# Kernel optimization log

Hardware: AMD Instinct MI355X
Metric: run time of the kernel (lower is better)

## Reference

```python
import jax, jax.numpy as jnp
import numpy as np
from jax import lax

C_OUT = 32   # out_capsules[0]
D_OUT = 8    # out_capsules[1]
ROUTING_ITERS = 3
EPS = 1e-8


def squash(s):
    # squash over capsule-channel axis c (dim 1 of B c d h w)
    n2 = jnp.sum(s * s, axis=1, keepdims=True)
    return s * (n2 / (1.0 + n2)) / jnp.sqrt(n2 + EPS)


def setup_inputs() -> dict:
    key = jax.random.key(0)
    k1, k2 = jax.random.split(key)
    x = jax.random.normal(k1, (8, 16, 8, 96, 96), dtype=jnp.float32)
    # torch Conv3d weight layout: (out_ch, in_ch, kD, kH, kW); scaled ~ kaiming-ish
    w_conv = jax.random.normal(k2, (C_OUT * D_OUT, 16, 1, 3, 3), dtype=jnp.float32) * 0.05
    return {"x": x, "w_conv": w_conv}


def reference(x, w_conv):
    # Conv3d, no bias, valid padding, stride 1, kernel (1,3,3)
    u = lax.conv_general_dilated(
        x, w_conv, window_strides=(1, 1, 1), padding='VALID',
        dimension_numbers=('NCDHW', 'OIDHW', 'NCDHW'))  # (B, c*d, D, h, w)
    B, _, D, h, w = u.shape
    # rearrange 'B (c d) D h w -> B c D d h w'
    u = u.reshape(B, C_OUT, D_OUT, D, h, w).transpose(0, 1, 3, 2, 4, 5)

    b = jnp.zeros((B, D, D_OUT, h, w), dtype=u.dtype)
    s = None
    for _ in range(ROUTING_ITERS):
        # softmax_3d: exp normalized over (d, h, w), keeping D
        e = jnp.exp(b)
        c = e / jnp.sum(e, axis=(2, 3, 4), keepdims=True)
        s = jnp.einsum('BDdhw,BcDdhw->Bcdhw', c, u)
        b = b + jnp.einsum('BcDdhw,Bcdhw->BDdhw', u, squash(s))
    return s
```

## Files before the change

kernel.cpp:

```cpp
#include <hip/hip_runtime.h>
#include <math.h>

#define CIN   16
#define DDEP  8
#define HIN   96
#define WIN   96
#define HOUT  94
#define WOUT  94
#define HW    (HOUT*WOUT)
#define CH    256
#define DCAP  8
#define KTOT  (CIN*9)
#define KTILES 5
#define APAD  168
#define EPSQ  1e-8f

#define B_ELEMS ((size_t)8*DDEP*DCAP*HW)
#define WFRAG_ELEMS ((size_t)KTILES*16*64*8)
#define BLK_PER_B (94*12)
#define NBLK ((size_t)8*BLK_PER_B)
#define A_TILE_BYTES ((size_t)64*APAD*2)
#define A_TILE_V4 (A_TILE_BYTES/16)
#define AC_BYTES (NBLK*A_TILE_BYTES)
#define VSITES (DCAP*HW)
#define NBLK2  277
#define G_BYTES ((size_t)8*VSITES*36*4)

typedef __attribute__((ext_vector_type(8))) short bf16x8;
typedef __attribute__((ext_vector_type(4))) float f32x4;

__device__ __forceinline__ ushort f2bf(float f) {
    unsigned u = __float_as_uint(f);
    return (ushort)((u + 0x7FFFu + ((u >> 16) & 1u)) >> 16);
}
__device__ __forceinline__ float bf2f(ushort h) {
    return __uint_as_float(((unsigned)h) << 16);
}

__global__ __launch_bounds__(64) void build_wfrag(
    const float* __restrict__ w, ushort* __restrict__ w_hi, ushort* __restrict__ w_lo)
{
    const int lane = threadIdx.x;
    const int nt = blockIdx.x, kt = blockIdx.y;
    const int n  = nt*16 + (lane & 15);
    const int kb = kt*32 + (lane >> 4)*8;
    size_t off = (((size_t)kt*16 + nt)*64 + lane)*8;
    for (int j = 0; j < 8; ++j) {
        int k = kb + j;
        float v = (k < KTOT) ? w[(size_t)n*KTOT + k] : 0.f;
        ushort hi = f2bf(v);
        float  r  = v - bf2f(hi);
        ushort lo = f2bf(r);
        w_hi[off + j] = hi; w_lo[off + j] = lo;
    }
}

__global__ __launch_bounds__(256) void zreduce(
    const float* __restrict__ Zp, float* __restrict__ Z, int dst, int count)
{
    const int bd = blockIdx.x;
    const float* p = Zp + (size_t)bd * count;
    float s = 0.f;
    for (int i = threadIdx.x; i < count; i += 256) s += p[i];
    #pragma unroll
    for (int off = 1; off < 64; off <<= 1) s += __shfl_xor(s, off);
    __shared__ float ps[4];
    if ((threadIdx.x & 63) == 0) ps[threadIdx.x >> 6] = s;
    __syncthreads();
    if (threadIdx.x == 0) Z[dst + bd] = ps[0] + ps[1] + ps[2] + ps[3];
}

template<int MODE>
__device__ __forceinline__ void routing_epilogue(
    const f32x4 (&acc)[4][4], const int t, const int wx, const int h0, const int bb,
    const float (*cms)[8], const float* invZ,
    float (*n2s)[8][8], float (*dbs)[8][8][8], float (*sout)[8],
    float* __restrict__ bws, float* __restrict__ Zp, float* __restrict__ out)
{
    const int w0 = wx*8;
    const int wv = t >> 6, lane = t & 63;
    const int m16 = lane & 15, quad = lane >> 4;
    const int d   = m16 & 7;
    const int Dq  = quad >> 1;
    const int wih = quad & 1;

    float svv[4][4];
    {
        float cmw[4][4];
        if (MODE == 0) {
            const float inv = 1.0f / (float)(DCAP * HW);
            #pragma unroll
            for (int mt = 0; mt < 4; ++mt)
                #pragma unroll
                for (int r = 0; r < 4; ++r) cmw[mt][r] = inv;
        } else {
            #pragma unroll
            for (int mt = 0; mt < 4; ++mt) {
                int D = mt*2 + Dq;
                float iz = invZ[D];
                #pragma unroll
                for (int r = 0; r < 4; ++r) cmw[mt][r] = cms[D*8 + d][wih*4 + r] * iz;
            }
        }
        #pragma unroll
        for (int nt = 0; nt < 4; ++nt)
            #pragma unroll
            for (int r = 0; r < 4; ++r) {
                float partial = 0.f;
                #pragma unroll
                for (int mt = 0; mt < 4; ++mt) partial += cmw[mt][r]*acc[mt][nt][r];
                partial += __shfl_xor(partial, 32);
                svv[nt][r] = partial;
            }
    }

    if (MODE == 2) {
        if (quad < 2) {
            #pragma unroll
            for (int nt = 0; nt < 4; ++nt) {
                int ch = wv*64 + nt*16 + m16;
                #pragma unroll
                for (int r = 0; r < 4; ++r) sout[ch][wih*4 + r] = svv[nt][r];
            }
        }
        __syncthreads();
        for (int i = t; i < 1024; i += 256) {
            int c2 = i >> 2, wip = i & 3;
            int w = w0 + wip*2;
            if (w + 1 < WOUT) {
                float2 v2 = { sout[c2][wip*2], sout[c2][wip*2 + 1] };
                *(float2*)&out[((size_t)bb*CH + c2)*HW + (size_t)h0*WOUT + w] = v2;
            }
        }
        return;
    }

    float p2[4];
    #pragma unroll
    for (int r = 0; r < 4; ++r) {
        float s2 = 0.f;
        #pragma unroll
        for (int nt = 0; nt < 4; ++nt) s2 += svv[nt][r]*svv[nt][r];
        p2[r] = s2;
    }
    #pragma unroll
    for (int r = 0; r < 4; ++r) p2[r] += __shfl_xor(p2[r], 8);
    if (quad < 2 && m16 < 8) {
        #pragma unroll
        for (int r = 0; r < 4; ++r) n2s[wv][m16][quad*4 + r] = p2[r];
    }
    __syncthreads();
    float fac[4];
    #pragma unroll
    for (int r = 0; r < 4; ++r) {
        int wi = wih*4 + r;
        float n2 = n2s[0][d][wi] + n2s[1][d][wi] + n2s[2][d][wi] + n2s[3][d][wi];
        fac[r] = (n2 / (1.f + n2)) / sqrtf(n2 + EPSQ);
    }
    float qv[4][4];
    #pragma unroll
    for (int mt = 0; mt < 4; ++mt)
        #pragma unroll
        for (int r = 0; r < 4; ++r) {
            float sum = 0.f;
            #pragma unroll
            for (int nt = 0; nt < 4; ++nt)
                sum += acc[mt][nt][r] * (svv[nt][r] * fac[r]);
            qv[mt][r] = sum;
        }
    #pragma unroll
    for (int mt = 0; mt < 4; ++mt)
        #pragma unroll
        for (int r = 0; r < 4; ++r) qv[mt][r] += __shfl_xor(qv[mt][r], 8);
    if (m16 < 8) {
        #pragma unroll
        for (int mt = 0; mt < 4; ++mt) {
            int D = mt*2 + Dq;
            #pragma unroll
            for (int r = 0; r < 4; ++r) dbs[wv][D][m16][wih*4 + r] = qv[mt][r];
        }
    }
    __syncthreads();
    {
        int Dd = t >> 2, wip = t & 3;
        int D = Dd >> 3, d2 = Dd & 7;
        int w = w0 + wip*2;
        float ez = 0.f;
        if (w + 1 < WOUT) {
            int wi = wip*2;
            float2 add;
            add.x = dbs[0][D][d2][wi]   + dbs[1][D][d2][wi]
                  + dbs[2][D][d2][wi]   + dbs[3][D][d2][wi];
            add.y = dbs[0][D][d2][wi+1] + dbs[1][D][d2][wi+1]
                  + dbs[2][D][d2][wi+1] + dbs[3][D][d2][wi+1];
            float2* bp = (float2*)&bws[((size_t)bb*64 + Dd)*HW + (size_t)h0*WOUT + w];
            if (MODE != 0) { float2 old = *bp; add.x += old.x; add.y += old.y; }
            *bp = add;
            ez = expf(add.x) + expf(add.y);
        }
        #pragma unroll
        for (int off = 1; off < 32; off <<= 1) ez += __shfl_xor(ez, off);
        if ((t & 31) == 0)
            Zp[((size_t)bb*8 + D)*BLK_PER_B + h0*12 + wx] = ez;
    }
}

template<int MODE, int AC, bool GW>
__global__ __launch_bounds__(256, 2) void conv_mfma_route(
    const float* __restrict__ x,
    const ushort* __restrict__ w_hi, const ushort* __restrict__ w_lo,
    float* __restrict__ bws, const float* __restrict__ Z,
    float* __restrict__ Zp, float* __restrict__ out,
    float* __restrict__ Ac, float* __restrict__ Gm)
{
    const int t  = threadIdx.x;
    const int wx = blockIdx.x, h0 = blockIdx.y, bb = blockIdx.z;
    const int w0 = wx*8;
    const size_t blk = ((size_t)bb*94 + h0)*12 + wx;

    __shared__ __align__(16) ushort a_hi[64][APAD];
    __shared__ float  cms[64][8];
    __shared__ float  invZ[8];
    __shared__ union {
        float patch[CIN][DDEP][3][10];
        struct { float n2s[4][8][8];
                 float dbs[4][8][8][8]; } ep;
        float sout[256][8];
        float gst[4][16][36];
    } ov;

    if (MODE != 0) {
        if (t < 8) invZ[t] = 1.0f / Z[(MODE == 2 ? 64 : 0) + bb*8 + t];
        for (int v = t; v < 512; v += 256) {
            int Dd = v >> 3, wi = v & 7;
            int w = w0 + wi;
            float bv = (w < WOUT) ? bws[((size_t)bb*64 + Dd)*HW + (size_t)h0*WOUT + w] : 0.f;
            cms[Dd][wi] = expf(bv);
        }
    }

    if (AC == 2) {
        const float4* src = (const float4*)Ac + blk*A_TILE_V4;
        float4* dst = (float4*)&a_hi[0][0];
        for (int i = t; i < A_TILE_V4; i += 256) dst[i] = src[i];
        __syncthreads();
    } else {
        for (int i = t; i < CIN*DDEP*3*10; i += 256) {
            int ci = i / 240, rem = i - ci*240;
            int D  = rem / 30, rem2 = rem - D*30;
            int kh = rem2 / 10, col = rem2 - kh*10;
            int xc = w0 + col; if (xc > 95) xc = 95;
            ov.patch[ci][D][kh][col] =
                x[(((size_t)(bb*CIN + ci)*DDEP + D)*HIN + (h0+kh))*WIN + xc];
        }
        __syncthreads();

        {
            const int site = t >> 2, kg = t & 3;
            const int D = site >> 3, wi = site & 7;
            #pragma unroll
            for (int u2 = 0; u2 < 18; ++u2) {
                int k0 = kg*36 + u2*2;
                int ci0 = k0/9, r0 = k0 - ci0*9, kh0 = r0/3, kw0 = r0 - kh0*3;
                int k1 = k0 + 1;
                int ci1 = k1/9, r1 = k1 - ci1*9, kh1 = r1/3, kw1 = r1 - kh1*3;
                unsigned lo = f2bf(ov.patch[ci0][D][kh0][wi+kw0]);
                unsigned hi = f2bf(ov.patch[ci1][D][kh1][wi+kw1]);
                *(unsigned*)&a_hi[site][k0] = lo | (hi << 16);
            }
            if (t < 64) {
                #pragma unroll
                for (int kk = KTOT; kk < KTILES*32; kk += 2)
                    *(unsigned*)&a_hi[t][kk] = 0u;
            }
        }
        __syncthreads();
    }

    const int wv = t >> 6, lane = t & 63;
    const int m16 = lane & 15, quad = lane >> 4;
    const int Dq = quad >> 1, wih = quad & 1;
    f32x4 acc[4][4];
    #pragma unroll
    for (int mt = 0; mt < 4; ++mt)
        #pragma unroll
        for (int nt = 0; nt < 4; ++nt)
            acc[mt][nt] = (f32x4){0.f, 0.f, 0.f, 0.f};

    #pragma unroll
    for (int kt = 0; kt < KTILES; ++kt) {
        bf16x8 ah[4];
        #pragma unroll
        for (int mt = 0; mt < 4; ++mt)
            ah[mt] = *(const bf16x8*)&a_hi[mt*16 + m16][kt*32 + quad*8];
        #pragma unroll
        for (int nt = 0; nt < 4; ++nt) {
            size_t off = (((size_t)kt*16 + (wv*4 + nt))*64 + lane)*8;
            bf16x8 bh = *(const bf16x8*)&w_hi[off];
            bf16x8 bl = *(const bf16x8*)&w_lo[off];
            #pragma unroll
            for (int mt = 0; mt < 4; ++mt) {
                acc[mt][nt] = __builtin_amdgcn_mfma_f32_16x16x32_bf16(ah[mt], bh, acc[mt][nt], 0, 0, 0);
                acc[mt][nt] = __builtin_amdgcn_mfma_f32_16x16x32_bf16(ah[mt], bl, acc[mt][nt], 0, 0, 0);
            }
        }
    }

    if (AC == 1) {
        float4* dst = (float4*)Ac + blk*A_TILE_V4;
        const float4* src = (const float4*)&a_hi[0][0];
        for (int i = t; i < A_TILE_V4; i += 256) dst[i] = src[i];
    }

    routing_epilogue<MODE>(acc, t, wx, h0, bb, cms, invZ,
                           ov.ep.n2s, ov.ep.dbs, ov.sout, bws, Zp, out);

    if constexpr (GW) {
        const int c3 = m16 >> 3;
        const int dL = m16 & 7;
        __syncthreads();
        #pragma unroll
        for (int r = 0; r < 4; ++r) {
            const int rq = r >> 1;
            float G36[36];
            #pragma unroll
            for (int j = 0; j < 36; ++j) G36[j] = 0.f;
            #pragma unroll
            for (int nt = 0; nt < 4; ++nt) {
                float u8[8];
                #pragma unroll
                for (int mt = 0; mt < 4; ++mt) {
                    float own = acc[mt][nt][r];
                    float oth = __shfl_xor(own, 32);
                    if (Dq == 0) { u8[mt*2]   = own; u8[mt*2+1] = oth; }
                    else         { u8[mt*2+1] = own; u8[mt*2]   = oth; }
                }
                if (Dq == rq) {
                    int idx = 0;
                    #pragma unroll
                    for (int D = 0; D < 8; ++D)
                        #pragma unroll
                        for (int Dp = D; Dp < 8; ++Dp) {
                            G36[idx] += u8[D]*u8[Dp];
                            ++idx;
                        }
                }
            }
            if (Dq == rq) {
                #pragma unroll
                for (int j = 0; j < 36; ++j) G36[j] += __shfl_xor(G36[j], 8);
                if (c3 == 0) {
                    #pragma unroll
                    for (int j = 0; j < 36; ++j) ov.gst[wv][dL*2 + wih][j] = G36[j];
                }
            }
            __syncthreads();
            for (int idx2 = t; idx2 < 16*36; idx2 += 256) {
                int sidx = idx2 / 36, j = idx2 - sidx*36;
                int dd = sidx >> 1, wh = sidx & 1;
                int w = w0 + wh*4 + r;
                if (w < WOUT) {
                    float gv = ov.gst[0][sidx][j] + ov.gst[1][sidx][j]
                             + ov.gst[2][sidx][j] + ov.gst[3][sidx][j];
                    size_t gsite = ((size_t)(bb*DCAP + dd)*HOUT + h0)*WOUT + w;
                    Gm[gsite*36 + j] = gv;
                }
            }
            __syncthreads();
        }
    }
}

__global__ __launch_bounds__(256) void gram_route(
    const float* __restrict__ Gm, float* __restrict__ bws,
    const float* __restrict__ Z, float* __restrict__ Zp)
{
    const int k = blockIdx.x, bb = blockIdx.y;
    const int t = threadIdx.x;
    const int local = k*256 + t;
    const bool valid = local < VSITES;
    float ez[8];
    #pragma unroll
    for (int D = 0; D < 8; ++D) ez[D] = 0.f;
    if (valid) {
        const int d  = local / HW;
        const int r2 = local - d*HW;
        float bv[8], cm[8];
        #pragma unroll
        for (int D = 0; D < 8; ++D) {
            bv[D] = bws[((size_t)(bb*64 + D*8 + d))*HW + r2];
            cm[D] = expf(bv[D]) * (1.0f / Z[bb*8 + D]);
        }
        float g[36];
        const float4* gp = (const float4*)(Gm + (size_t)(bb*VSITES + local)*36);
        #pragma unroll
        for (int q = 0; q < 9; ++q) {
            float4 v = gp[q];
            g[q*4+0] = v.x; g[q*4+1] = v.y; g[q*4+2] = v.z; g[q*4+3] = v.w;
        }
        float tD[8];
        #pragma unroll
        for (int D = 0; D < 8; ++D) tD[D] = 0.f;
        {
            int idx = 0;
            #pragma unroll
            for (int D = 0; D < 8; ++D)
                #pragma unroll
                for (int Dp = D; Dp < 8; ++Dp) {
                    float gv = g[idx]; ++idx;
                    tD[D] += cm[Dp] * gv;
                    if (Dp != D) tD[Dp] += cm[D] * gv;
                }
        }
        float n2 = 0.f;
        #pragma unroll
        for (int D = 0; D < 8; ++D) n2 += cm[D] * tD[D];
        float fac = (n2 / (1.f + n2)) / sqrtf(n2 + EPSQ);
        #pragma unroll
        for (int D = 0; D < 8; ++D) {
            float nb = bv[D] + fac * tD[D];
            bws[((size_t)(bb*64 + D*8 + d))*HW + r2] = nb;
            ez[D] = expf(nb);
        }
    }
    #pragma unroll
    for (int D = 0; D < 8; ++D)
        #pragma unroll
        for (int off = 1; off < 64; off <<= 1) ez[D] += __shfl_xor(ez[D], off);
    __shared__ float ps[4][8];
    if ((t & 63) == 0) {
        #pragma unroll
        for (int D = 0; D < 8; ++D) ps[t >> 6][D] = ez[D];
    }
    __syncthreads();
    if (t < 8)
        Zp[((size_t)bb*8 + t)*NBLK2 + k] = ps[0][t] + ps[1][t] + ps[2][t] + ps[3][t];
}

extern "C" void kernel_launch(void* const* d_in, const int* in_sizes, int n_in,
                              void* d_out, int out_size, void* d_ws, size_t ws_size,
                              hipStream_t stream)
{
    (void)in_sizes; (void)n_in; (void)out_size;
    const float* x     = (const float*)d_in[0];
    const float* wconv = (const float*)d_in[1];
    float* out = (float*)d_out;

    float*  bws  = (float*)d_ws;
    float*  Z    = bws + B_ELEMS;
    float*  Zp   = Z + 128;
    ushort* w_hi = (ushort*)(Zp + 64*BLK_PER_B);
    ushort* w_lo = w_hi + WFRAG_ELEMS;
    size_t  base = (size_t)((char*)(w_lo + WFRAG_ELEMS) - (char*)d_ws);
    size_t  goff = (base + 255) & ~(size_t)255;
    float*  Gm   = (float*)((char*)d_ws + goff);
    size_t  aoff = (goff + G_BYTES + 255) & ~(size_t)255;
    float*  Ac   = (float*)((char*)d_ws + aoff);
    const bool haveG = ws_size >= goff + G_BYTES;
    const bool haveA = ws_size >= aoff + AC_BYTES;

    const dim3 grid(12, 94, 8);
    build_wfrag<<<dim3(16, KTILES), 64, 0, stream>>>(wconv, w_hi, w_lo);
    if (haveG && haveA) {
        conv_mfma_route<0, 1, true ><<<grid, 256, 0, stream>>>(x, w_hi, w_lo, bws, Z, Zp, out, Ac, Gm);
        zreduce<<<64, 256, 0, stream>>>(Zp, Z, 0, BLK_PER_B);
        gram_route<<<dim3(NBLK2, 8), 256, 0, stream>>>(Gm, bws, Z, Zp);
        zreduce<<<64, 256, 0, stream>>>(Zp, Z, 64, NBLK2);
        conv_mfma_route<2, 2, false><<<grid, 256, 0, stream>>>(x, w_hi, w_lo, bws, Z, Zp, out, Ac, nullptr);
    } else if (haveG) {
        conv_mfma_route<0, 0, true ><<<grid, 256, 0, stream>>>(x, w_hi, w_lo, bws, Z, Zp, out, nullptr, Gm);
        zreduce<<<64, 256, 0, stream>>>(Zp, Z, 0, BLK_PER_B);
        gram_route<<<dim3(NBLK2, 8), 256, 0, stream>>>(Gm, bws, Z, Zp);
        zreduce<<<64, 256, 0, stream>>>(Zp, Z, 64, NBLK2);
        conv_mfma_route<2, 0, false><<<grid, 256, 0, stream>>>(x, w_hi, w_lo, bws, Z, Zp, out, nullptr, nullptr);
    } else {
        conv_mfma_route<0, 0, false><<<grid, 256, 0, stream>>>(x, w_hi, w_lo, bws, Z, Zp, out, nullptr, nullptr);
        zreduce<<<64, 256, 0, stream>>>(Zp, Z, 0, BLK_PER_B);
        conv_mfma_route<1, 0, false><<<grid, 256, 0, stream>>>(x, w_hi, w_lo, bws, Z, Zp, out, nullptr, nullptr);
        zreduce<<<64, 256, 0, stream>>>(Zp, Z, 64, BLK_PER_B);
        conv_mfma_route<2, 0, false><<<grid, 256, 0, stream>>>(x, w_hi, w_lo, bws, Z, Zp, out, nullptr, nullptr);
    }
}
```

Before: 592.0 us.

## Route all iterations through Gram matrices and pre-convert input to bf16

Pre-converts x to bf16 once in a separate kernel so both conv passes load half-width patches. The first conv pass now only computes per-site 8x8 Gram matrices (no routing epilogue or A-tile caching), and iteration one's routing update is moved into a templated gram_route with uniform coupling. A dedicated final conv kernel computes the weighted sum output, and occupancy is raised to 4 blocks per SM. The workspace-size fallbacks are removed, so the path assumes enough workspace for xb and Gm.

After: 1.401 ms. 2.37x slower.

```diff
diff --git a/kernel.cpp b/kernel.cpp
--- a/kernel.cpp
+++ b/kernel.cpp
@@ -17,13 +17,9 @@
 
 #define B_ELEMS ((size_t)8*DDEP*DCAP*HW)
 #define WFRAG_ELEMS ((size_t)KTILES*16*64*8)
-#define BLK_PER_B (94*12)
-#define NBLK ((size_t)8*BLK_PER_B)
-#define A_TILE_BYTES ((size_t)64*APAD*2)
-#define A_TILE_V4 (A_TILE_BYTES/16)
-#define AC_BYTES (NBLK*A_TILE_BYTES)
 #define VSITES (DCAP*HW)
 #define NBLK2  277
+#define XN ((size_t)8*CIN*DDEP*HIN*WIN)
 #define G_BYTES ((size_t)8*VSITES*36*4)
 
 typedef __attribute__((ext_vector_type(8))) short bf16x8;
@@ -55,6 +51,17 @@
     }
 }
 
+__global__ __launch_bounds__(256) void xconvert(
+    const float* __restrict__ x, ushort* __restrict__ xb)
+{
+    size_t i = (size_t)blockIdx.x*256 + threadIdx.x;
+    if (i*4 >= XN) return;
+    float4 v = ((const float4*)x)[i];
+    ushort4 o;
+    o.x = f2bf(v.x); o.y = f2bf(v.y); o.z = f2bf(v.z); o.w = f2bf(v.w);
+    ((ushort4*)xb)[i] = o;
+}
+
 __global__ __launch_bounds__(256) void zreduce(
     const float* __restrict__ Zp, float* __restrict__ Z, int dst, int count)
 {
@@ -70,212 +77,54 @@
     if (threadIdx.x == 0) Z[dst + bd] = ps[0] + ps[1] + ps[2] + ps[3];
 }
 
-template<int MODE>
-__device__ __forceinline__ void routing_epilogue(
-    const f32x4 (&acc)[4][4], const int t, const int wx, const int h0, const int bb,
-    const float (*cms)[8], const float* invZ,
-    float (*n2s)[8][8], float (*dbs)[8][8][8], float (*sout)[8],
-    float* __restrict__ bws, float* __restrict__ Zp, float* __restrict__ out)
-{
-    const int w0 = wx*8;
-    const int wv = t >> 6, lane = t & 63;
-    const int m16 = lane & 15, quad = lane >> 4;
-    const int d   = m16 & 7;
-    const int Dq  = quad >> 1;
-    const int wih = quad & 1;
-
-    float svv[4][4];
-    {
-        float cmw[4][4];
-        if (MODE == 0) {
-            const float inv = 1.0f / (float)(DCAP * HW);
-            #pragma unroll
-            for (int mt = 0; mt < 4; ++mt)
-                #pragma unroll
-                for (int r = 0; r < 4; ++r) cmw[mt][r] = inv;
-        } else {
-            #pragma unroll
-            for (int mt = 0; mt < 4; ++mt) {
-                int D = mt*2 + Dq;
-                float iz = invZ[D];
-                #pragma unroll
-                for (int r = 0; r < 4; ++r) cmw[mt][r] = cms[D*8 + d][wih*4 + r] * iz;
-            }
-        }
-        #pragma unroll
-        for (int nt = 0; nt < 4; ++nt)
-            #pragma unroll
-            for (int r = 0; r < 4; ++r) {
-                float partial = 0.f;
-                #pragma unroll
-                for (int mt = 0; mt < 4; ++mt) partial += cmw[mt][r]*acc[mt][nt][r];
-                partial += __shfl_xor(partial, 32);
-                svv[nt][r] = partial;
-            }
-    }
-
-    if (MODE == 2) {
-        if (quad < 2) {
-            #pragma unroll
-            for (int nt = 0; nt < 4; ++nt) {
-                int ch = wv*64 + nt*16 + m16;
-                #pragma unroll
-                for (int r = 0; r < 4; ++r) sout[ch][wih*4 + r] = svv[nt][r];
-            }
-        }
-        __syncthreads();
-        for (int i = t; i < 1024; i += 256) {
-            int c2 = i >> 2, wip = i & 3;
-            int w = w0 + wip*2;
-            if (w + 1 < WOUT) {
-                float2 v2 = { sout[c2][wip*2], sout[c2][wip*2 + 1] };
-                *(float2*)&out[((size_t)bb*CH + c2)*HW + (size_t)h0*WOUT + w] = v2;
-            }
-        }
-        return;
-    }
-
-    float p2[4];
-    #pragma unroll
-    for (int r = 0; r < 4; ++r) {
-        float s2 = 0.f;
-        #pragma unroll
-        for (int nt = 0; nt < 4; ++nt) s2 += svv[nt][r]*svv[nt][r];
-        p2[r] = s2;
-    }
-    #pragma unroll
-    for (int r = 0; r < 4; ++r) p2[r] += __shfl_xor(p2[r], 8);
-    if (quad < 2 && m16 < 8) {
-        #pragma unroll
-        for (int r = 0; r < 4; ++r) n2s[wv][m16][quad*4 + r] = p2[r];
-    }
-    __syncthreads();
-    float fac[4];
-    #pragma unroll
-    for (int r = 0; r < 4; ++r) {
-        int wi = wih*4 + r;
-        float n2 = n2s[0][d][wi] + n2s[1][d][wi] + n2s[2][d][wi] + n2s[3][d][wi];
-        fac[r] = (n2 / (1.f + n2)) / sqrtf(n2 + EPSQ);
-    }
-    float qv[4][4];
-    #pragma unroll
-    for (int mt = 0; mt < 4; ++mt)
-        #pragma unroll
-        for (int r = 0; r < 4; ++r) {
-            float sum = 0.f;
-            #pragma unroll
-            for (int nt = 0; nt < 4; ++nt)
-                sum += acc[mt][nt][r] * (svv[nt][r] * fac[r]);
-            qv[mt][r] = sum;
-        }
-    #pragma unroll
-    for (int mt = 0; mt < 4; ++mt)
-        #pragma unroll
-        for (int r = 0; r < 4; ++r) qv[mt][r] += __shfl_xor(qv[mt][r], 8);
-    if (m16 < 8) {
-        #pragma unroll
-        for (int mt = 0; mt < 4; ++mt) {
-            int D = mt*2 + Dq;
-            #pragma unroll
-            for (int r = 0; r < 4; ++r) dbs[wv][D][m16][wih*4 + r] = qv[mt][r];
-        }
-    }
-    __syncthreads();
-    {
-        int Dd = t >> 2, wip = t & 3;
-        int D = Dd >> 3, d2 = Dd & 7;
-        int w = w0 + wip*2;
-        float ez = 0.f;
-        if (w + 1 < WOUT) {
-            int wi = wip*2;
-            float2 add;
-            add.x = dbs[0][D][d2][wi]   + dbs[1][D][d2][wi]
-                  + dbs[2][D][d2][wi]   + dbs[3][D][d2][wi];
-            add.y = dbs[0][D][d2][wi+1] + dbs[1][D][d2][wi+1]
-                  + dbs[2][D][d2][wi+1] + dbs[3][D][d2][wi+1];
-            float2* bp = (float2*)&bws[((size_t)bb*64 + Dd)*HW + (size_t)h0*WOUT + w];
-            if (MODE != 0) { float2 old = *bp; add.x += old.x; add.y += old.y; }
-            *bp = add;
-            ez = expf(add.x) + expf(add.y);
-        }
-        #pragma unroll
-        for (int off = 1; off < 32; off <<= 1) ez += __shfl_xor(ez, off);
-        if ((t & 31) == 0)
-            Zp[((size_t)bb*8 + D)*BLK_PER_B + h0*12 + wx] = ez;
-    }
-}
-
-template<int MODE, int AC, bool GW>
-__global__ __launch_bounds__(256, 2) void conv_mfma_route(
-    const float* __restrict__ x,
+__global__ __launch_bounds__(256, 4) void conv_g(
+    const ushort* __restrict__ xb,
     const ushort* __restrict__ w_hi, const ushort* __restrict__ w_lo,
-    float* __restrict__ bws, const float* __restrict__ Z,
-    float* __restrict__ Zp, float* __restrict__ out,
-    float* __restrict__ Ac, float* __restrict__ Gm)
+    float* __restrict__ Gm)
 {
     const int t  = threadIdx.x;
     const int wx = blockIdx.x, h0 = blockIdx.y, bb = blockIdx.z;
     const int w0 = wx*8;
-    const size_t blk = ((size_t)bb*94 + h0)*12 + wx;
 
     __shared__ __align__(16) ushort a_hi[64][APAD];
-    __shared__ float  cms[64][8];
-    __shared__ float  invZ[8];
     __shared__ union {
-        float patch[CIN][DDEP][3][10];
-        struct { float n2s[4][8][8];
-                 float dbs[4][8][8][8]; } ep;
-        float sout[256][8];
-        float gst[4][16][36];
+        ushort patchb[CIN][DDEP][3][10];
+        float  gst[2][4][16][36];
     } ov;
 
-    if (MODE != 0) {
-        if (t < 8) invZ[t] = 1.0f / Z[(MODE == 2 ? 64 : 0) + bb*8 + t];
-        for (int v = t; v < 512; v += 256) {
-            int Dd = v >> 3, wi = v & 7;
-            int w = w0 + wi;
-            float bv = (w < WOUT) ? bws[((size_t)bb*64 + Dd)*HW + (size_t)h0*WOUT + w] : 0.f;
-            cms[Dd][wi] = expf(bv);
-        }
-    }
-
-    if (AC == 2) {
-        const float4* src = (const float4*)Ac + blk*A_TILE_V4;
-        float4* dst = (float4*)&a_hi[0][0];
-        for (int i = t; i < A_TILE_V4; i += 256) dst[i] = src[i];
-        __syncthreads();
-    } else {
-        for (int i = t; i < CIN*DDEP*3*10; i += 256) {
-            int ci = i / 240, rem = i - ci*240;
-            int D  = rem / 30, rem2 = rem - D*30;
-            int kh = rem2 / 10, col = rem2 - kh*10;
-            int xc = w0 + col; if (xc > 95) xc = 95;
-            ov.patch[ci][D][kh][col] =
-                x[(((size_t)(bb*CIN + ci)*DDEP + D)*HIN + (h0+kh))*WIN + xc];
-        }
-        __syncthreads();
-
-        {
-            const int site = t >> 2, kg = t & 3;
-            const int D = site >> 3, wi = site & 7;
-            #pragma unroll
-            for (int u2 = 0; u2 < 18; ++u2) {
-                int k0 = kg*36 + u2*2;
-                int ci0 = k0/9, r0 = k0 - ci0*9, kh0 = r0/3, kw0 = r0 - kh0*3;
-                int k1 = k0 + 1;
-                int ci1 = k1/9, r1 = k1 - ci1*9, kh1 = r1/3, kw1 = r1 - kh1*3;
-                unsigned lo = f2bf(ov.patch[ci0][D][kh0][wi+kw0]);
-                unsigned hi = f2bf(ov.patch[ci1][D][kh1][wi+kw1]);
-                *(unsigned*)&a_hi[site][k0] = lo | (hi << 16);
-            }
-            if (t < 64) {
-                #pragma unroll
-                for (int kk = KTOT; kk < KTILES*32; kk += 2)
-                    *(unsigned*)&a_hi[t][kk] = 0u;
-            }
-        }
-        __syncthreads();
-    }
+    for (int i = t; i < CIN*DDEP*3*5; i += 256) {
+        int ci = i / 120, rem = i - ci*120;
+        int D  = rem / 15, r2 = rem - D*15;
+        int kh = r2 / 5, uc = r2 - kh*5;
+        int xc = w0 + uc*2;
+        const ushort* row = xb + (((size_t)(bb*CIN + ci)*DDEP + D)*HIN + (h0+kh))*WIN;
+        unsigned v;
+        if (xc + 1 < WIN) v = *(const unsigned*)&row[xc];
+        else { unsigned e = row[95]; v = e | (e << 16); }
+        *(unsigned*)&ov.patchb[ci][D][kh][uc*2] = v;
+    }
+    __syncthreads();
+
+    {
+        const int site = t >> 2, kg = t & 3;
+        const int D = site >> 3, wi = site & 7;
+        #pragma unroll
+        for (int u2 = 0; u2 < 18; ++u2) {
+            int k0 = kg*36 + u2*2;
+            int ci0 = k0/9, r0 = k0 - ci0*9, kh0 = r0/3, kw0 = r0 - kh0*3;
+            int k1 = k0 + 1;
+            int ci1 = k1/9, r1 = k1 - ci1*9, kh1 = r1/3, kw1 = r1 - kh1*3;
+            unsigned lo = ov.patchb[ci0][D][kh0][wi+kw0];
+            unsigned hi = ov.patchb[ci1][D][kh1][wi+kw1];
+            *(unsigned*)&a_hi[site][k0] = lo | (hi << 16);
+        }
+        if (t < 64) {
+            #pragma unroll
+            for (int kk = KTOT; kk < KTILES*32; kk += 2)
+                *(unsigned*)&a_hi[t][kk] = 0u;
+        }
+    }
+    __syncthreads();
 
     const int wv = t >> 6, lane = t & 63;
     const int m16 = lane & 15, quad = lane >> 4;
@@ -306,22 +155,12 @@
         }
     }
 
-    if (AC == 1) {
-        float4* dst = (float4*)Ac + blk*A_TILE_V4;
-        const float4* src = (const float4*)&a_hi[0][0];
-        for (int i = t; i < A_TILE_V4; i += 256) dst[i] = src[i];
-    }
-
-    routing_epilogue<MODE>(acc, t, wx, h0, bb, cms, invZ,
-                           ov.ep.n2s, ov.ep.dbs, ov.sout, bws, Zp, out);
-
-    if constexpr (GW) {
-        const int c3 = m16 >> 3;
-        const int dL = m16 & 7;
-        __syncthreads();
-        #pragma unroll
-        for (int r = 0; r < 4; ++r) {
-            const int rq = r >> 1;
+    const int dL = m16 & 7;
+    #pragma unroll
+    for (int rp = 0; rp < 2; ++rp) {
+        #pragma unroll
+        for (int rb = 0; rb < 2; ++rb) {
+            const int r = rp*2 + rb;
             float G36[36];
             #pragma unroll
             for (int j = 0; j < 36; ++j) G36[j] = 0.f;
@@ -332,45 +171,43 @@
                 for (int mt = 0; mt < 4; ++mt) {
                     float own = acc[mt][nt][r];
                     float oth = __shfl_xor(own, 32);
-                    if (Dq == 0) { u8[mt*2]   = own; u8[mt*2+1] = oth; }
-                    else         { u8[mt*2+1] = own; u8[mt*2]   = oth; }
+                    u8[mt*2]     = (Dq == 0) ? own : oth;
+                    u8[mt*2 + 1] = (Dq == 0) ? oth : own;
                 }
-                if (Dq == rq) {
-                    int idx = 0;
+                int idx = 0;
+                #pragma unroll
+                for (int D = 0; D < 8; ++D)
                     #pragma unroll
-                    for (int D = 0; D < 8; ++D)
-                        #pragma unroll
-                        for (int Dp = D; Dp < 8; ++Dp) {
-                            G36[idx] += u8[D]*u8[Dp];
-                            ++idx;
-                        }
-                }
-            }
-            if (Dq == rq) {
+                    for (int Dp = D; Dp < 8; ++Dp) {
+                        G36[idx] += u8[D]*u8[Dp];
+                        ++idx;
+                    }
+            }
+            #pragma unroll
+            for (int j = 0; j < 36; ++j) G36[j] += __shfl_xor(G36[j], 8);
+            if (Dq == 0 && m16 < 8) {
                 #pragma unroll
-                for (int j = 0; j < 36; ++j) G36[j] += __shfl_xor(G36[j], 8);
-                if (c3 == 0) {
-                    #pragma unroll
-                    for (int j = 0; j < 36; ++j) ov.gst[wv][dL*2 + wih][j] = G36[j];
-                }
-            }
-            __syncthreads();
-            for (int idx2 = t; idx2 < 16*36; idx2 += 256) {
-                int sidx = idx2 / 36, j = idx2 - sidx*36;
-                int dd = sidx >> 1, wh = sidx & 1;
-                int w = w0 + wh*4 + r;
-                if (w < WOUT) {
-                    float gv = ov.gst[0][sidx][j] + ov.gst[1][sidx][j]
-                             + ov.gst[2][sidx][j] + ov.gst[3][sidx][j];
-                    size_t gsite = ((size_t)(bb*DCAP + dd)*HOUT + h0)*WOUT + w;
-                    Gm[gsite*36 + j] = gv;
-                }
-            }
-            __syncthreads();
-        }
-    }
-}
-
+                for (int j = 0; j < 36; ++j) ov.gst[rb][wv][dL*2 + wih][j] = G36[j];
+            }
+        }
+        __syncthreads();
+        for (int idx2 = t; idx2 < 2*16*36; idx2 += 256) {
+            int rb = idx2 / 576, rem = idx2 - rb*576;
+            int sidx = rem / 36, j = rem - sidx*36;
+            int dd = sidx >> 1, wh = sidx & 1;
+            int w = w0 + wh*4 + rp*2 + rb;
+            if (w < WOUT) {
+                float gv = ov.gst[rb][0][sidx][j] + ov.gst[rb][1][sidx][j]
+                         + ov.gst[rb][2][sidx][j] + ov.gst[rb][3][sidx][j];
+                size_t gsite = ((size_t)(bb*DCAP + dd)*HOUT + h0)*WOUT + w;
+                Gm[gsite*36 + j] = gv;
+            }
+        }
+        if (rp == 0) __syncthreads();
+    }
+}
+
+template<int ITER>
 __global__ __launch_bounds__(256) void gram_route(
     const float* __restrict__ Gm, float* __restrict__ bws,
     const float* __restrict__ Z, float* __restrict__ Zp)
@@ -379,17 +216,23 @@
     const int t = threadIdx.x;
     const int local = k*256 + t;
     const bool valid = local < VSITES;
-    float ez[8];
-    #pragma unroll
-    for (int D = 0; D < 8; ++D) ez[D] = 0.f;
+    float ez8[8];
+    #pragma unroll
+    for (int D = 0; D < 8; ++D) ez8[D] = 0.f;
     if (valid) {
         const int d  = local / HW;
         const int r2 = local - d*HW;
         float bv[8], cm[8];
-        #pragma unroll
-        for (int D = 0; D < 8; ++D) {
-            bv[D] = bws[((size_t)(bb*64 + D*8 + d))*HW + r2];
-            cm[D] = expf(bv[D]) * (1.0f / Z[bb*8 + D]);
+        if (ITER == 1) {
+            const float inv = 1.0f / (float)(DCAP * HW);
+            #pragma unroll
+            for (int D = 0; D < 8; ++D) { bv[D] = 0.f; cm[D] = inv; }
+        } else {
+            #pragma unroll
+            for (int D = 0; D < 8; ++D) {
+                bv[D] = bws[((size_t)(bb*64 + D*8 + d))*HW + r2];
+                cm[D] = expf(bv[D]) * (1.0f / Z[bb*8 + D]);
+            }
         }
         float g[36];
         const float4* gp = (const float4*)(Gm + (size_t)(bb*VSITES + local)*36);
@@ -420,28 +263,158 @@
         for (int D = 0; D < 8; ++D) {
             float nb = bv[D] + fac * tD[D];
             bws[((size_t)(bb*64 + D*8 + d))*HW + r2] = nb;
-            ez[D] = expf(nb);
+            ez8[D] = expf(nb);
         }
     }
     #pragma unroll
     for (int D = 0; D < 8; ++D)
         #pragma unroll
-        for (int off = 1; off < 64; off <<= 1) ez[D] += __shfl_xor(ez[D], off);
+        for (int off = 1; off < 64; off <<= 1) ez8[D] += __shfl_xor(ez8[D], off);
     __shared__ float ps[4][8];
     if ((t & 63) == 0) {
         #pragma unroll
-        for (int D = 0; D < 8; ++D) ps[t >> 6][D] = ez[D];
+        for (int D = 0; D < 8; ++D) ps[t >> 6][D] = ez8[D];
     }
     __syncthreads();
     if (t < 8)
         Zp[((size_t)bb*8 + t)*NBLK2 + k] = ps[0][t] + ps[1][t] + ps[2][t] + ps[3][t];
+}
+
+__global__ __launch_bounds__(256, 4) void conv_s(
+    const ushort* __restrict__ xb,
+    const ushort* __restrict__ w_hi, const ushort* __restrict__ w_lo,
+    const float* __restrict__ bws, const float* __restrict__ Z,
+    float* __restrict__ out)
+{
+    const int t  = threadIdx.x;
+    const int wx = blockIdx.x, h0 = blockIdx.y, bb = blockIdx.z;
+    const int w0 = wx*8;
+
+    __shared__ __align__(16) ushort a_hi[64][APAD];
+    __shared__ float  cms[64][8];
+    __shared__ float  invZ[8];
+    __shared__ union {
+        ushort patchb[CIN][DDEP][3][10];
+        float  sout[256][8];
+    } ov;
+
+    if (t < 8) invZ[t] = 1.0f / Z[64 + bb*8 + t];
+    for (int v = t; v < 512; v += 256) {
+        int Dd = v >> 3, wi = v & 7;
+        int w = w0 + wi;
+        float bv = (w < WOUT) ? bws[((size_t)bb*64 + Dd)*HW + (size_t)h0*WOUT + w] : 0.f;
+        cms[Dd][wi] = expf(bv);
+    }
+    for (int i = t; i < CIN*DDEP*3*5; i += 256) {
+        int ci = i / 120, rem = i - ci*120;
+        int D  = rem / 15, r2 = rem - D*15;
+        int kh = r2 / 5, uc = r2 - kh*5;
+        int xc = w0 + uc*2;
+        const ushort* row = xb + (((size_t)(bb*CIN + ci)*DDEP + D)*HIN + (h0+kh))*WIN;
+        unsigned v;
+        if (xc + 1 < WIN) v = *(const unsigned*)&row[xc];
+        else { unsigned e = row[95]; v = e | (e << 16); }
+        *(unsigned*)&ov.patchb[ci][D][kh][uc*2] = v;
+    }
+    __syncthreads();
+
+    {
+        const int site = t >> 2, kg = t & 3;
+        const int D = site >> 3, wi = site & 7;
+        #pragma unroll
+        for (int u2 = 0; u2 < 18; ++u2) {
+            int k0 = kg*36 + u2*2;
+            int ci0 = k0/9, r0 = k0 - ci0*9, kh0 = r0/3, kw0 = r0 - kh0*3;
+            int k1 = k0 + 1;
+            int ci1 = k1/9, r1 = k1 - ci1*9, kh1 = r1/3, kw1 = r1 - kh1*3;
+            unsigned lo = ov.patchb[ci0][D][kh0][wi+kw0];
+            unsigned hi = ov.patchb[ci1][D][kh1][wi+kw1];
+            *(unsigned*)&a_hi[site][k0] = lo | (hi << 16);
+        }
+        if (t < 64) {
+            #pragma unroll
+            for (int kk = KTOT; kk < KTILES*32; kk += 2)
+                *(unsigned*)&a_hi[t][kk] = 0u;
+        }
+    }
+    __syncthreads();
+
+    const int wv = t >> 6, lane = t & 63;
+    const int m16 = lane & 15, quad = lane >> 4;
+    f32x4 acc[4][4];
+    #pragma unroll
+    for (int mt = 0; mt < 4; ++mt)
+        #pragma unroll
+        for (int nt = 0; nt < 4; ++nt)
+            acc[mt][nt] = (f32x4){0.f, 0.f, 0.f, 0.f};
+
+    #pragma unroll
+    for (int kt = 0; kt < KTILES; ++kt) {
+        bf16x8 ah[4];
+        #pragma unroll
+        for (int mt = 0; mt < 4; ++mt)
+            ah[mt] = *(const bf16x8*)&a_hi[mt*16 + m16][kt*32 + quad*8];
+        #pragma unroll
+        for (int nt = 0; nt < 4; ++nt) {
+            size_t off = (((size_t)kt*16 + (wv*4 + nt))*64 + lane)*8;
+            bf16x8 bh = *(const bf16x8*)&w_hi[off];
+            bf16x8 bl = *(const bf16x8*)&w_lo[off];
+            #pragma unroll
+            for (int mt = 0; mt < 4; ++mt) {
+                acc[mt][nt] = __builtin_amdgcn_mfma_f32_16x16x32_bf16(ah[mt], bh, acc[mt][nt], 0, 0, 0);
+                acc[mt][nt] = __builtin_amdgcn_mfma_f32_16x16x32_bf16(ah[mt], bl, acc[mt][nt], 0, 0, 0);
+            }
+        }
+    }
+
+    const int d   = m16 & 7;
+    const int Dq  = quad >> 1;
+    const int wih = quad & 1;
+    float svv[4][4];
+    {
+        float cmw[4][4];
+        #pragma unroll
+        for (int mt = 0; mt < 4; ++mt) {
+            int D = mt*2 + Dq;
+            float iz = invZ[D];
+            #pragma unroll
+            for (int r = 0; r < 4; ++r) cmw[mt][r] = cms[D*8 + d][wih*4 + r] * iz;
+        }
+        #pragma unroll
+        for (int nt = 0; nt < 4; ++nt)
+            #pragma unroll
+            for (int r = 0; r < 4; ++r) {
+                float partial = 0.f;
+                #pragma unroll
+                for (int mt = 0; mt < 4; ++mt) partial += cmw[mt][r]*acc[mt][nt][r];
+                partial += __shfl_xor(partial, 32);
+                svv[nt][r] = partial;
+            }
+    }
+    if (quad < 2) {
+        #pragma unroll
+        for (int nt = 0; nt < 4; ++nt) {
+            int ch = wv*64 + nt*16 + m16;
+            #pragma unroll
+            for (int r = 0; r < 4; ++r) ov.sout[ch][wih*4 + r] = svv[nt][r];
+        }
+    }
+    __syncthreads();
+    for (int i = t; i < 1024; i += 256) {
+        int c2 = i >> 2, wip = i & 3;
+        int w = w0 + wip*2;
+        if (w + 1 < WOUT) {
+            float2 v2 = { ov.sout[c2][wip*2], ov.sout[c2][wip*2 + 1] };
+            *(float2*)&out[((size_t)bb*CH + c2)*HW + (size_t)h0*WOUT + w] = v2;
+        }
+    }
 }
 
 extern "C" void kernel_launch(void* const* d_in, const int* in_sizes, int n_in,
                               void* d_out, int out_size, void* d_ws, size_t ws_size,
                               hipStream_t stream)
 {
-    (void)in_sizes; (void)n_in; (void)out_size;
+    (void)in_sizes; (void)n_in; (void)out_size; (void)ws_size;
     const float* x     = (const float*)d_in[0];
     const float* wconv = (const float*)d_in[1];
     float* out = (float*)d_out;
@@ -449,35 +422,20 @@
     float*  bws  = (float*)d_ws;
     float*  Z    = bws + B_ELEMS;
     float*  Zp   = Z + 128;
-    ushort* w_hi = (ushort*)(Zp + 64*BLK_PER_B);
+    ushort* w_hi = (ushort*)(Zp + 64*NBLK2);
     ushort* w_lo = w_hi + WFRAG_ELEMS;
-    size_t  base = (size_t)((char*)(w_lo + WFRAG_ELEMS) - (char*)d_ws);
+    ushort* xb   = w_lo + WFRAG_ELEMS;
+    size_t  base = (size_t)((char*)(xb + XN) - (char*)d_ws);
     size_t  goff = (base + 255) & ~(size_t)255;
     float*  Gm   = (float*)((char*)d_ws + goff);
-    size_t  aoff = (goff + G_BYTES + 255) & ~(size_t)255;
-    float*  Ac   = (float*)((char*)d_ws + aoff);
-    const bool haveG = ws_size >= goff + G_BYTES;
-    const bool haveA = ws_size >= aoff + AC_BYTES;
 
     const dim3 grid(12, 94, 8);
     build_wfrag<<<dim3(16, KTILES), 64, 0, stream>>>(wconv, w_hi, w_lo);
-    if (haveG && haveA) {
-        conv_mfma_route<0, 1, true ><<<grid, 256, 0, stream>>>(x, w_hi, w_lo, bws, Z, Zp, out, Ac, Gm);
-        zreduce<<<64, 256, 0, stream>>>(Zp, Z, 0, BLK_PER_B);
-        gram_route<<<dim3(NBLK2, 8), 256, 0, stream>>>(Gm, bws, Z, Zp);
-        zreduce<<<64, 256, 0, stream>>>(Zp, Z, 64, NBLK2);
-        conv_mfma_route<2, 2, false><<<grid, 256, 0, stream>>>(x, w_hi, w_lo, bws, Z, Zp, out, Ac, nullptr);
-    } else if (haveG) {
-        conv_mfma_route<0, 0, true ><<<grid, 256, 0, stream>>>(x, w_hi, w_lo, bws, Z, Zp, out, nullptr, Gm);
-        zreduce<<<64, 256, 0, stream>>>(Zp, Z, 0, BLK_PER_B);
-        gram_route<<<dim3(NBLK2, 8), 256, 0, stream>>>(Gm, bws, Z, Zp);
-        zreduce<<<64, 256, 0, stream>>>(Zp, Z, 64, NBLK2);
-        conv_mfma_route<2, 0, false><<<grid, 256, 0, stream>>>(x, w_hi, w_lo, bws, Z, Zp, out, nullptr, nullptr);
-    } else {
-        conv_mfma_route<0, 0, false><<<grid, 256, 0, stream>>>(x, w_hi, w_lo, bws, Z, Zp, out, nullptr, nullptr);
-        zreduce<<<64, 256, 0, stream>>>(Zp, Z, 0, BLK_PER_B);
-        conv_mfma_route<1, 0, false><<<grid, 256, 0, stream>>>(x, w_hi, w_lo, bws, Z, Zp, out, nullptr, nullptr);
-        zreduce<<<64, 256, 0, stream>>>(Zp, Z, 64, BLK_PER_B);
-        conv_mfma_route<2, 0, false><<<grid, 256, 0, stream>>>(x, w_hi, w_lo, bws, Z, Zp, out, nullptr, nullptr);
-    }
-}
+    xconvert<<<(unsigned)(XN/4/256), 256, 0, stream>>>(x, xb);
+    conv_g<<<grid, 256, 0, stream>>>(xb, w_hi, w_lo, Gm);
+    gram_route<1><<<dim3(NBLK2, 8), 256, 0, stream>>>(Gm, bws, Z, Zp);
+    zreduce<<<64, 256, 0, stream>>>(Zp, Z, 0, NBLK2);
+    gram_route<2><<<dim3(NBLK2, 8), 256, 0, stream>>>(Gm, bws, Z, Zp);
+    zreduce<<<64, 256, 0, stream>>>(Zp, Z, 64, NBLK2);
+    conv_s<<<grid, 256, 0, stream>>>(xb, w_hi, w_lo, bws, Z, out);
+}
```
